# Kernel tuning notes

Measured on AMD Instinct MI355X. Metric: run time of the kernel, lower is better.

Reference implementation:

```python
import jax, jax.numpy as jnp
import numpy as np

HPC = 42  # HPC_FEATURES_LEN

def setup_inputs() -> dict:
    key = jax.random.key(0)
    ks = jax.random.split(key, 8)
    B, N, C, P, S = 4, 16384, 103, 2048, 32
    xyz = jax.random.normal(ks[0], (B, N, 3), dtype=jnp.float32)
    features = jax.random.normal(ks[1], (B, C, N), dtype=jnp.float32)
    new_xyz = jax.random.normal(ks[2], (B, P, 3), dtype=jnp.float32)
    idx = jax.random.randint(ks[3], (B, P, S), 0, N, dtype=jnp.int32)
    # 1x1-conv weights (out_ch, in_ch); gate conv sees full 3+C=106 channels
    Wg = jax.random.normal(ks[4], (64, 106), dtype=jnp.float32) * 0.05
    bg = jnp.zeros((64,), dtype=jnp.float32)
    W1 = jax.random.normal(ks[5], (64, 64), dtype=jnp.float32) * 0.05
    b1 = jnp.zeros((64,), dtype=jnp.float32)
    W2 = jax.random.normal(ks[6], (128, 64), dtype=jnp.float32) * 0.05
    b2 = jnp.zeros((128,), dtype=jnp.float32)
    W3 = jax.random.normal(ks[7], (256, 128), dtype=jnp.float32) * 0.05
    b3 = jnp.zeros((256,), dtype=jnp.float32)
    return {"xyz": xyz, "features": features, "new_xyz": new_xyz, "idx": idx,
            "Wg": Wg, "bg": bg, "W1": W1, "b1": b1, "W2": W2, "b2": b2,
            "W3": W3, "b3": b3}

def reference(xyz, features, new_xyz, idx, Wg, bg, W1, b1, W2, b2, W3, b3):
    # --- grouping: gather neighbors, center xyz, concat features ---
    # grouped_xyz: (B, P, S, 3) -> (B, 3, P, S)
    grouped_xyz = jax.vmap(lambda x, i: x[i])(xyz, idx) - new_xyz[:, :, None, :]
    grouped_xyz = jnp.transpose(grouped_xyz, (0, 3, 1, 2))
    # grouped_feat: (B, C, P, S)
    grouped_feat = jax.vmap(lambda f, i: f[:, i])(features, idx)
    nf = jnp.concatenate([grouped_xyz, grouped_feat], axis=1)  # (B, 3+C, P, S)
    base = nf[:, :-HPC]                                        # (B, 3+C-42, P, S)
    # --- gating 1x1 conv on full channels, then elementwise gate ---
    w = jnp.einsum('bcps,oc->bops', nf, Wg) + bg[None, :, None, None]
    x = base * (1.0 + w)
    # --- 1x1-conv MLP stack with ReLU ---
    for W, b in ((W1, b1), (W2, b2), (W3, b3)):
        x = jax.nn.relu(jnp.einsum('bcps,oc->bops', x, W) + b[None, :, None, None])
    # --- max pool over nsample ---
    pooled = jnp.max(x, axis=-1)  # (B, 256, P)
    return new_xyz, pooled
```

## Files before the change

### kernel.cpp

```cpp
#include <hip/hip_runtime.h>
#include <stdint.h>


namespace {
constexpr int kB = 4, kN = 16384, kC = 103, kP = 2048, kS = 32;

using short8 = __attribute__((ext_vector_type(8))) short;
using short4 = __attribute__((ext_vector_type(4))) short;
using f32x4  = __attribute__((ext_vector_type(4))) float;

constexpr int WG_HI = 0,     WG_LO = 8192;
constexpr int W1_HI = 16384, W1_LO = 20480;
constexpr int W2_HI = 24576, W2_LO = 32768;
constexpr int W3_HI = 40960, W3_LO = 73728;
constexpr size_t FT_OFF    = 262144;
constexpr size_t FT_SHORTS = (size_t)kB * kN * 128;
constexpr size_t WS_NEED   = FT_OFF + 2 * FT_SHORTS * 2;

__device__ __forceinline__ unsigned short f2bf(float x) {
    unsigned u = __float_as_uint(x);
    u += 0x7fffu + ((u >> 16) & 1u);
    return (unsigned short)(u >> 16);
}
__device__ __forceinline__ float bf2f(unsigned short h) {
    return __uint_as_float((unsigned)h << 16);
}

__global__ void copy_newxyz(const float* __restrict__ src, float* __restrict__ dst, int n) {
    int i = blockIdx.x * blockDim.x + threadIdx.x;
    if (i < n) dst[i] = src[i];
}

__global__ void prep_weights(const float* __restrict__ Wg, const float* __restrict__ W1,
                             const float* __restrict__ W2, const float* __restrict__ W3,
                             short* __restrict__ ws) {
    int i = blockIdx.x * blockDim.x + threadIdx.x;
    if (i >= 53248) return;
    float w; int hi, lo, j;
    if (i < 8192)       { j = i;         int o = j >> 7, c = j & 127; w = (c < 106) ? Wg[o * 106 + c] : 0.f; hi = WG_HI; lo = WG_LO; }
    else if (i < 12288) { j = i - 8192;  int o = j >> 6, c = j & 63;  w = W1[o * 64 + c];  hi = W1_HI; lo = W1_LO; }
    else if (i < 20480) { j = i - 12288; int o = j >> 6, c = j & 63;  w = W2[o * 64 + c];  hi = W2_HI; lo = W2_LO; }
    else                { j = i - 20480; int o = j >> 7, c = j & 127; w = W3[o * 128 + c]; hi = W3_HI; lo = W3_LO; }
    unsigned short h = f2bf(w);
    ws[hi + j] = (short)h;
    ws[lo + j] = (short)f2bf(w - bf2f(h));
}

__global__ __launch_bounds__(512) void prep_feat(const float* __restrict__ f,
                                                 short* __restrict__ ftH, short* __restrict__ ftL) {
    __shared__ float tile[kC][65];
    const int bb = blockIdx.x >> 8;
    const int n0 = (blockIdx.x & 255) * 64;
    const int tid = threadIdx.x;
    for (int c = tid >> 6; c < kC; c += 8)
        tile[c][tid & 63] = f[((size_t)bb * kC + c) * kN + n0 + (tid & 63)];
    __syncthreads();
    const int np = tid >> 3, gc = tid & 7;
    short* rH = ftH + ((size_t)bb * kN + n0 + np) * 128;
    short* rL = ftL + ((size_t)bb * kN + n0 + np) * 128;
    #pragma unroll
    for (int kk = 0; kk < 2; ++kk) {
        const int chunk = gc + 8 * kk;
        union { uint4 u; short s[8]; } H, L;
        #pragma unroll
        for (int e = 0; e < 8; ++e) {
            const int col = chunk * 8 + e;
            float v = (col >= 3 && col < 106) ? tile[col - 3][np] : 0.f;
            unsigned short hh = f2bf(v);
            H.s[e] = (short)hh;
            L.s[e] = (short)f2bf(v - bf2f(hh));
        }
        *(uint4*)(rH + chunk * 8) = H.u;
        *(uint4*)(rL + chunk * 8) = L.u;
    }
}

template<int NOT, int NPT, int KT, int LDC>
__device__ __forceinline__ void gemm_stage(
    const short* __restrict__ xh, const short* __restrict__ xl,
    const short* __restrict__ wh, const short* __restrict__ wl,
    const float* __restrict__ bias,
    int ot0, int pt0t, int lane, f32x4 (&acc)[NOT][NPT])
{
    const int q = lane >> 4, n16 = lane & 15;
    #pragma unroll
    for (int i = 0; i < NOT; ++i) {
        const f32x4 binit = *(const f32x4*)(bias + (ot0 + i) * 16 + 4 * q);
        #pragma unroll
        for (int j = 0; j < NPT; ++j) acc[i][j] = binit;
    }
    #pragma unroll
    for (int kt = 0; kt < KT; ++kt) {
        const int k0 = kt * 32 + q * 8;
        short8 bh[NPT], bl[NPT];
        #pragma unroll
        for (int j = 0; j < NPT; ++j) {
            const int p = (pt0t + j) * 16 + n16;
            const int e = p * LDC + (k0 ^ ((p & 7) << 3));
            bh[j] = *(const short8*)(xh + e);
            bl[j] = *(const short8*)(xl + e);
        }
        #pragma unroll
        for (int i = 0; i < NOT; ++i) {
            const size_t we = (size_t)((ot0 + i) * 16 + n16) * (KT * 32) + k0;
            const short8 ah = *(const short8*)(wh + we);
            const short8 al = *(const short8*)(wl + we);
            #pragma unroll
            for (int j = 0; j < NPT; ++j) {
                acc[i][j] = __builtin_amdgcn_mfma_f32_16x16x32_bf16(ah, bh[j], acc[i][j], 0, 0, 0);
                acc[i][j] = __builtin_amdgcn_mfma_f32_16x16x32_bf16(ah, bl[j], acc[i][j], 0, 0, 0);
                acc[i][j] = __builtin_amdgcn_mfma_f32_16x16x32_bf16(al, bh[j], acc[i][j], 0, 0, 0);
            }
        }
    }
}

template<int NOT, int NPT, bool GATE, int LDCO>
__device__ __forceinline__ void store_act(
    f32x4 (&acc)[NOT][NPT], short* __restrict__ oh, short* __restrict__ ol,
    const short* __restrict__ nfh, const short* __restrict__ nfl,
    int ot0, int pt0t, int lane)
{
    const int q = lane >> 4, n16 = lane & 15;
    #pragma unroll
    for (int i = 0; i < NOT; ++i) {
        const int ob = (ot0 + i) * 16 + 4 * q;
        #pragma unroll
        for (int j = 0; j < NPT; ++j) {
            const int p = (pt0t + j) * 16 + n16;
            const int cs = ob ^ ((p & 7) << 3);
            float v[4];
            #pragma unroll
            for (int r = 0; r < 4; ++r) v[r] = acc[i][j][r];
            if (GATE) {
                const short4 h4 = *(const short4*)(nfh + p * 128 + cs);
                const short4 l4 = *(const short4*)(nfl + p * 128 + cs);
                #pragma unroll
                for (int r = 0; r < 4; ++r) {
                    const float base = bf2f((unsigned short)h4[r]) + bf2f((unsigned short)l4[r]);
                    v[r] = fmaf(base, v[r], base);
                }
            } else {
                #pragma unroll
                for (int r = 0; r < 4; ++r) v[r] = fmaxf(v[r], 0.f);
            }
            short4 h4o, l4o;
            #pragma unroll
            for (int r = 0; r < 4; ++r) {
                const unsigned short h = f2bf(v[r]);
                h4o[r] = (short)h;
                l4o[r] = (short)f2bf(v[r] - bf2f(h));
            }
            *(short4*)(oh + p * LDCO + cs) = h4o;
            *(short4*)(ol + p * LDCO + cs) = l4o;
        }
    }
}

template<bool DENSE>
__global__ __launch_bounds__(512, 4) void pointnet_sa(
    const float* __restrict__ xyz, const float* __restrict__ features,
    const float* __restrict__ new_xyz, const int* __restrict__ idx,
    const short* __restrict__ ws, const short* __restrict__ ftH, const short* __restrict__ ftL,
    const float* __restrict__ bg, const float* __restrict__ b1,
    const float* __restrict__ b2, const float* __restrict__ b3,
    float* __restrict__ out_pooled)
{
    __shared__ short smem[32768];
    short* NFh = smem;          short* NFl = smem + 8192;
    short* X0h = smem + 16384;  short* X0l = smem + 20480;
    short* X1h = smem + 24576;  short* X1l = smem + 28672;
    short* X2h = NFh;           short* X2l = NFl;

    const int tid = threadIdx.x, lane = tid & 63, wave = tid >> 6;
    const int q = lane >> 4, n16 = lane & 15;
    const int pt0 = blockIdx.x * 64;
    const int b = pt0 >> 16;

    if (DENSE) {
        const int gp = tid >> 3, gc = tid & 7;
        const int pt = pt0 + gp;
        const int n = idx[pt];
        const short* rH = ftH + ((size_t)b * kN + n) * 128;
        const short* rL = ftL + ((size_t)b * kN + n) * 128;
        uint4 hc0 = *(const uint4*)(rH + gc * 8);
        uint4 hc1 = *(const uint4*)(rH + gc * 8 + 64);
        uint4 lc0 = *(const uint4*)(rL + gc * 8);
        uint4 lc1 = *(const uint4*)(rL + gc * 8 + 64);
        if (gc == 0) {
            const float* xp = xyz + ((size_t)b * kN + n) * 3;
            const int pp = (pt >> 5) & (kP - 1);
            const float* np = new_xyz + ((size_t)b * kP + pp) * 3;
            union { uint4 u; short s[8]; } H, L;
            H.u = hc0; L.u = lc0;
            #pragma unroll
            for (int c = 0; c < 3; ++c) {
                const float v = xp[c] - np[c];
                const unsigned short hh = f2bf(v);
                H.s[c] = (short)hh;
                L.s[c] = (short)f2bf(v - bf2f(hh));
            }
            hc0 = H.u; lc0 = L.u;
        }
        const int sw = (gc ^ (gp & 7)) * 8;
        *(uint4*)(NFh + gp * 128 + sw)      = hc0;
        *(uint4*)(NFh + gp * 128 + sw + 64) = hc1;
        *(uint4*)(NFl + gp * 128 + sw)      = lc0;
        *(uint4*)(NFl + gp * 128 + sw + 64) = lc1;
    } else {
        const int p = tid & 63;
        const int cg = tid >> 6;
        const int pt = pt0 + p;
        const int n = idx[pt];
        const int pp = (pt >> 5) & (kP - 1);
        const float* fb = features + (size_t)b * kC * kN + n;
        const float* xp = xyz + ((size_t)b * kN + n) * 3;
        const float* np = new_xyz + ((size_t)b * kP + pp) * 3;
        for (int c = cg; c < 128; c += 8) {
            float v;
            if (c < 3)        v = xp[c] - np[c];
            else if (c < 106) v = fb[(size_t)(c - 3) * kN];
            else              v = 0.f;
            const unsigned short h = f2bf(v);
            const int cs = c ^ ((p & 7) << 3);
            NFh[p * 128 + cs] = (short)h;
            NFl[p * 128 + cs] = (short)f2bf(v - bf2f(h));
        }
    }
    __syncthreads();

    {
        f32x4 acc[1][2];
        gemm_stage<1, 2, 4, 128>(NFh, NFl, ws + WG_HI, ws + WG_LO, bg,
                                 wave & 3, 2 * (wave >> 2), lane, acc);
        store_act<1, 2, true, 64>(acc, X0h, X0l, NFh, NFl, wave & 3, 2 * (wave >> 2), lane);
    }
    __syncthreads();

    {
        f32x4 acc[1][2];
        gemm_stage<1, 2, 2, 64>(X0h, X0l, ws + W1_HI, ws + W1_LO, b1,
                                wave & 3, 2 * (wave >> 2), lane, acc);
        store_act<1, 2, false, 64>(acc, X1h, X1l, nullptr, nullptr, wave & 3, 2 * (wave >> 2), lane);
    }
    __syncthreads();

    {
        f32x4 acc[2][2];
        gemm_stage<2, 2, 2, 64>(X1h, X1l, ws + W2_HI, ws + W2_LO, b2,
                                2 * (wave & 3), 2 * (wave >> 2), lane, acc);
        store_act<2, 2, false, 128>(acc, X2h, X2l, nullptr, nullptr, 2 * (wave & 3), 2 * (wave >> 2), lane);
    }
    __syncthreads();

    {
        f32x4 acc[2][4];
        gemm_stage<2, 4, 4, 128>(X2h, X2l, ws + W3_HI, ws + W3_LO, b3,
                                 2 * wave, 0, lane, acc);
        #pragma unroll
        for (int i = 0; i < 2; ++i) {
            #pragma unroll
            for (int sg = 0; sg < 2; ++sg) {
                #pragma unroll
                for (int r = 0; r < 4; ++r) {
                    float a = fmaxf(acc[i][2 * sg][r], acc[i][2 * sg + 1][r]);
                    a = fmaxf(a, __shfl_xor(a, 1, 16));
                    a = fmaxf(a, __shfl_xor(a, 2, 16));
                    a = fmaxf(a, __shfl_xor(a, 4, 16));
                    a = fmaxf(a, __shfl_xor(a, 8, 16));
                    a = fmaxf(a, 0.f);
                    if (n16 == 0) {
                        const int o = (2 * wave + i) * 16 + 4 * q + r;
                        const int g = (pt0 >> 5) + sg;
                        out_pooled[((size_t)(g >> 11) * 256 + o) * kP + (g & (kP - 1))] = a;
                    }
                }
            }
        }
    }
}
}

extern "C" void kernel_launch(void* const* d_in, const int* in_sizes, int n_in,
                              void* d_out, int out_size, void* d_ws, size_t ws_size,
                              hipStream_t stream) {
    const float* xyz      = (const float*)d_in[0];
    const float* features = (const float*)d_in[1];
    const float* new_xyz  = (const float*)d_in[2];
    const int*   idx      = (const int*)d_in[3];
    const float* Wg = (const float*)d_in[4];
    const float* bg = (const float*)d_in[5];
    const float* W1 = (const float*)d_in[6];
    const float* b1 = (const float*)d_in[7];
    const float* W2 = (const float*)d_in[8];
    const float* b2 = (const float*)d_in[9];
    const float* W3 = (const float*)d_in[10];
    const float* b3 = (const float*)d_in[11];
    float* out = (float*)d_out;
    short* ws  = (short*)d_ws;
    short* ftH = (short*)((char*)d_ws + FT_OFF);
    short* ftL = ftH + FT_SHORTS;

    const int nxyz = kB * kP * 3;
    copy_newxyz<<<(nxyz + 255) / 256, 256, 0, stream>>>(new_xyz, out, nxyz);
    prep_weights<<<(53248 + 255) / 256, 256, 0, stream>>>(Wg, W1, W2, W3, ws);

    float* pooled = out + nxyz;
    if (ws_size >= WS_NEED) {
        prep_feat<<<kB * (kN / 64), 512, 0, stream>>>(features, ftH, ftL);
        pointnet_sa<true><<<(kB * kP * kS) / 64, 512, 0, stream>>>(
            xyz, features, new_xyz, idx, ws, ftH, ftL, bg, b1, b2, b3, pooled);
    } else {
        pointnet_sa<false><<<(kB * kP * kS) / 64, 512, 0, stream>>>(
            xyz, features, new_xyz, idx, ws, nullptr, nullptr, bg, b1, b2, b3, pooled);
    }
}
```

Before: 185.9 us.

## Pipeline neighbor gathers via direct-to-LDS loads across multiple tiles per block

```diff
diff --git a/kernel.cpp b/kernel.cpp
--- a/kernel.cpp
+++ b/kernel.cpp
@@ -2,8 +2,12 @@
 #include <stdint.h>
 
 
+#define AS1 __attribute__((address_space(1)))
+#define AS3 __attribute__((address_space(3)))
+
 namespace {
 constexpr int kB = 4, kN = 16384, kC = 103, kP = 2048, kS = 32;
+constexpr int TPB = 4;
 
 using short8 = __attribute__((ext_vector_type(8))) short;
 using short4 = __attribute__((ext_vector_type(4))) short;
@@ -24,6 +28,14 @@
 }
 __device__ __forceinline__ float bf2f(unsigned short h) {
     return __uint_as_float((unsigned)h << 16);
+}
+
+__device__ __forceinline__ void glds16(const short* g, short* l) {
+    __builtin_amdgcn_global_load_lds((const AS1 unsigned int*)g, (AS3 unsigned int*)l, 16, 0, 0);
+}
+__device__ __forceinline__ void wg_barrier() {
+    asm volatile("s_waitcnt lgkmcnt(0)" ::: "memory");
+    __builtin_amdgcn_s_barrier();
 }
 
 __global__ void copy_newxyz(const float* __restrict__ src, float* __restrict__ dst, int n) {
@@ -111,6 +123,36 @@
                 acc[i][j] = __builtin_amdgcn_mfma_f32_16x16x32_bf16(ah, bl[j], acc[i][j], 0, 0, 0);
                 acc[i][j] = __builtin_amdgcn_mfma_f32_16x16x32_bf16(al, bh[j], acc[i][j], 0, 0, 0);
             }
+        }
+    }
+}
+
+template<int NPT, int KT, int LDC>
+__device__ __forceinline__ void gemm_pre(
+    const short* __restrict__ xh, const short* __restrict__ xl,
+    const short8* ah, const short8* al, const float* __restrict__ bias,
+    int ot0, int pt0t, int lane, f32x4 (&acc)[1][NPT])
+{
+    const int q = lane >> 4, n16 = lane & 15;
+    const f32x4 binit = *(const f32x4*)(bias + ot0 * 16 + 4 * q);
+    #pragma unroll
+    for (int j = 0; j < NPT; ++j) acc[0][j] = binit;
+    #pragma unroll
+    for (int kt = 0; kt < KT; ++kt) {
+        const int k0 = kt * 32 + q * 8;
+        short8 bh[NPT], bl[NPT];
+        #pragma unroll
+        for (int j = 0; j < NPT; ++j) {
+            const int p = (pt0t + j) * 16 + n16;
+            const int e = p * LDC + (k0 ^ ((p & 7) << 3));
+            bh[j] = *(const short8*)(xh + e);
+            bl[j] = *(const short8*)(xl + e);
+        }
+        #pragma unroll
+        for (int j = 0; j < NPT; ++j) {
+            acc[0][j] = __builtin_amdgcn_mfma_f32_16x16x32_bf16(ah[kt], bh[j], acc[0][j], 0, 0, 0);
+            acc[0][j] = __builtin_amdgcn_mfma_f32_16x16x32_bf16(ah[kt], bl[j], acc[0][j], 0, 0, 0);
+            acc[0][j] = __builtin_amdgcn_mfma_f32_16x16x32_bf16(al[kt], bh[j], acc[0][j], 0, 0, 0);
         }
     }
 }
@@ -157,16 +199,180 @@
     }
 }
 
-template<bool DENSE>
-__global__ __launch_bounds__(512, 4) void pointnet_sa(
-    const float* __restrict__ xyz, const float* __restrict__ features,
-    const float* __restrict__ new_xyz, const int* __restrict__ idx,
+__global__ __launch_bounds__(512, 4) void pointnet_sa_pipe(
+    const float* __restrict__ xyz, const float* __restrict__ new_xyz,
+    const int* __restrict__ idx,
     const short* __restrict__ ws, const short* __restrict__ ftH, const short* __restrict__ ftL,
     const float* __restrict__ bg, const float* __restrict__ b1,
     const float* __restrict__ b2, const float* __restrict__ b3,
     float* __restrict__ out_pooled)
 {
-    __shared__ short smem[32768];
+    __shared__ alignas(16) short smem[32768];
+    __shared__ alignas(16) float biasL[512];
+    short* NFh = smem;          short* NFl = smem + 8192;
+    short* X0h = smem + 16384;  short* X0l = smem + 20480;
+    short* X1h = smem + 24576;  short* X1l = smem + 28672;
+    short* X2h = smem + 16384;  short* X2l = smem + 24576;
+
+    const int tid = threadIdx.x, lane = tid & 63, wave = tid >> 6;
+    const int q = lane >> 4, n16 = lane & 15;
+    const int base = blockIdx.x * (64 * TPB);
+    const int b = base >> 16;
+    const size_t fb = (size_t)b * kN * 128;
+
+    biasL[tid] = (tid < 64) ? bg[tid] : (tid < 128) ? b1[tid - 64]
+               : (tid < 256) ? b2[tid - 128] : b3[tid - 256];
+
+    short8 w1h2[2], w1l2[2];
+    {
+        const int row = (wave & 3) * 16 + n16;
+        #pragma unroll
+        for (int kt = 0; kt < 2; ++kt) {
+            w1h2[kt] = *(const short8*)(ws + W1_HI + row * 64 + kt * 32 + q * 8);
+            w1l2[kt] = *(const short8*)(ws + W1_LO + row * 64 + kt * 32 + q * 8);
+        }
+    }
+
+    {
+        const int r0 = wave * 8 + (lane >> 4);
+        const int n0 = idx[base + r0];
+        const int n1 = idx[base + r0 + 4];
+        const int c0 = ((lane & 15) ^ (lane >> 4)) * 8;
+        const int c1 = ((lane & 15) ^ (4 + (lane >> 4))) * 8;
+        const int l0 = __builtin_amdgcn_readfirstlane(wave * 1024);
+        glds16(ftH + fb + (size_t)n0 * 128 + c0, smem + l0);
+        glds16(ftH + fb + (size_t)n1 * 128 + c1, smem + l0 + 512);
+        glds16(ftL + fb + (size_t)n0 * 128 + c0, smem + 8192 + l0);
+        glds16(ftL + fb + (size_t)n1 * 128 + c1, smem + 8192 + l0 + 512);
+    }
+    float xr0 = 0, xr1 = 0, xr2 = 0, nx0 = 0, nx1 = 0, nx2 = 0;
+    if ((lane & 7) == 0) {
+        const int p = wave * 8 + (lane >> 3);
+        const int n = idx[base + p];
+        const float* xp = xyz + ((size_t)b * kN + n) * 3;
+        const int pp = ((base + p) >> 5) & (kP - 1);
+        const float* np = new_xyz + ((size_t)b * kP + pp) * 3;
+        xr0 = xp[0]; xr1 = xp[1]; xr2 = xp[2];
+        nx0 = np[0]; nx1 = np[1]; nx2 = np[2];
+    }
+    __syncthreads();
+    if ((lane & 7) == 0) {
+        const int p = wave * 8 + (lane >> 3);
+        const int o = p * 128 + (p & 7) * 8;
+        float xd[3] = { xr0 - nx0, xr1 - nx1, xr2 - nx2 };
+        #pragma unroll
+        for (int c = 0; c < 3; ++c) {
+            const unsigned short h = f2bf(xd[c]);
+            NFh[o + c] = (short)h;
+            NFl[o + c] = (short)f2bf(xd[c] - bf2f(h));
+        }
+    }
+    wg_barrier();
+
+    for (int t = 0; t < TPB; ++t) {
+        const int tb = base + t * 64;
+        int ni0 = 0, ni1 = 0, nxy = 0;
+        if (t + 1 < TPB) {
+            const int r0 = wave * 8 + (lane >> 4);
+            ni0 = idx[tb + 64 + r0];
+            ni1 = idx[tb + 64 + r0 + 4];
+            if ((lane & 7) == 0) nxy = idx[tb + 64 + wave * 8 + (lane >> 3)];
+        }
+
+        {
+            f32x4 a0[1][2];
+            gemm_stage<1, 2, 4, 128>(NFh, NFl, ws + WG_HI, ws + WG_LO, biasL,
+                                     wave & 3, 2 * (wave >> 2), lane, a0);
+            store_act<1, 2, true, 64>(a0, X0h, X0l, NFh, NFl, wave & 3, 2 * (wave >> 2), lane);
+        }
+        wg_barrier();
+
+        if (t + 1 < TPB) {
+            const int c0 = ((lane & 15) ^ (lane >> 4)) * 8;
+            const int c1 = ((lane & 15) ^ (4 + (lane >> 4))) * 8;
+            const int l0 = __builtin_amdgcn_readfirstlane(wave * 1024);
+            glds16(ftH + fb + (size_t)ni0 * 128 + c0, smem + l0);
+            glds16(ftH + fb + (size_t)ni1 * 128 + c1, smem + l0 + 512);
+            glds16(ftL + fb + (size_t)ni0 * 128 + c0, smem + 8192 + l0);
+            glds16(ftL + fb + (size_t)ni1 * 128 + c1, smem + 8192 + l0 + 512);
+            if ((lane & 7) == 0) {
+                const int p = wave * 8 + (lane >> 3);
+                const float* xp = xyz + ((size_t)b * kN + nxy) * 3;
+                const int pp = ((tb + 64 + p) >> 5) & (kP - 1);
+                const float* np = new_xyz + ((size_t)b * kP + pp) * 3;
+                xr0 = xp[0]; xr1 = xp[1]; xr2 = xp[2];
+                nx0 = np[0]; nx1 = np[1]; nx2 = np[2];
+            }
+        }
+
+        {
+            f32x4 a1[1][2];
+            gemm_pre<2, 2, 64>(X0h, X0l, w1h2, w1l2, biasL + 64,
+                               wave & 3, 2 * (wave >> 2), lane, a1);
+            store_act<1, 2, false, 64>(a1, X1h, X1l, nullptr, nullptr,
+                                       wave & 3, 2 * (wave >> 2), lane);
+        }
+        wg_barrier();
+
+        f32x4 a2[2][2];
+        gemm_stage<2, 2, 2, 64>(X1h, X1l, ws + W2_HI, ws + W2_LO, biasL + 128,
+                                2 * (wave & 3), 2 * (wave >> 2), lane, a2);
+        wg_barrier();
+        store_act<2, 2, false, 128>(a2, X2h, X2l, nullptr, nullptr,
+                                    2 * (wave & 3), 2 * (wave >> 2), lane);
+        wg_barrier();
+
+        {
+            f32x4 a3[2][4];
+            gemm_stage<2, 4, 4, 128>(X2h, X2l, ws + W3_HI, ws + W3_LO, biasL + 256,
+                                     2 * wave, 0, lane, a3);
+            #pragma unroll
+            for (int i = 0; i < 2; ++i)
+                #pragma unroll
+                for (int sg = 0; sg < 2; ++sg)
+                    #pragma unroll
+                    for (int r = 0; r < 4; ++r) {
+                        float a = fmaxf(a3[i][2 * sg][r], a3[i][2 * sg + 1][r]);
+                        a = fmaxf(a, __shfl_xor(a, 1, 16));
+                        a = fmaxf(a, __shfl_xor(a, 2, 16));
+                        a = fmaxf(a, __shfl_xor(a, 4, 16));
+                        a = fmaxf(a, __shfl_xor(a, 8, 16));
+                        a = fmaxf(a, 0.f);
+                        if (n16 == 0) {
+                            const int o = (2 * wave + i) * 16 + 4 * q + r;
+                            const int g = (tb >> 5) + sg;
+                            out_pooled[((size_t)(g >> 11) * 256 + o) * kP + (g & (kP - 1))] = a;
+                        }
+                    }
+        }
+
+        if (t + 1 < TPB) {
+            asm volatile("s_waitcnt vmcnt(0)" ::: "memory");
+            if ((lane & 7) == 0) {
+                const int p = wave * 8 + (lane >> 3);
+                const int o = p * 128 + (p & 7) * 8;
+                float xd[3] = { xr0 - nx0, xr1 - nx1, xr2 - nx2 };
+                #pragma unroll
+                for (int c = 0; c < 3; ++c) {
+                    const unsigned short h = f2bf(xd[c]);
+                    NFh[o + c] = (short)h;
+                    NFl[o + c] = (short)f2bf(xd[c] - bf2f(h));
+                }
+            }
+            wg_barrier();
+        }
+    }
+}
+
+__global__ __launch_bounds__(512, 4) void pointnet_sa_scalar(
+    const float* __restrict__ xyz, const float* __restrict__ features,
+    const float* __restrict__ new_xyz, const int* __restrict__ idx,
+    const short* __restrict__ ws,
+    const float* __restrict__ bg, const float* __restrict__ b1,
+    const float* __restrict__ b2, const float* __restrict__ b3,
+    float* __restrict__ out_pooled)
+{
+    __shared__ alignas(16) short smem[32768];
     short* NFh = smem;          short* NFl = smem + 8192;
     short* X0h = smem + 16384;  short* X0l = smem + 20480;
     short* X1h = smem + 24576;  short* X1l = smem + 28672;
@@ -177,49 +383,19 @@
     const int pt0 = blockIdx.x * 64;
     const int b = pt0 >> 16;
 
-    if (DENSE) {
-        const int gp = tid >> 3, gc = tid & 7;
-        const int pt = pt0 + gp;
-        const int n = idx[pt];
-        const short* rH = ftH + ((size_t)b * kN + n) * 128;
-        const short* rL = ftL + ((size_t)b * kN + n) * 128;
-        uint4 hc0 = *(const uint4*)(rH + gc * 8);
-        uint4 hc1 = *(const uint4*)(rH + gc * 8 + 64);
-        uint4 lc0 = *(const uint4*)(rL + gc * 8);
-        uint4 lc1 = *(const uint4*)(rL + gc * 8 + 64);
-        if (gc == 0) {
-            const float* xp = xyz + ((size_t)b * kN + n) * 3;
-            const int pp = (pt >> 5) & (kP - 1);
-            const float* np = new_xyz + ((size_t)b * kP + pp) * 3;
-            union { uint4 u; short s[8]; } H, L;
-            H.u = hc0; L.u = lc0;
-            #pragma unroll
-            for (int c = 0; c < 3; ++c) {
-                const float v = xp[c] - np[c];
-                const unsigned short hh = f2bf(v);
-                H.s[c] = (short)hh;
-                L.s[c] = (short)f2bf(v - bf2f(hh));
-            }
-            hc0 = H.u; lc0 = L.u;
-        }
-        const int sw = (gc ^ (gp & 7)) * 8;
-        *(uint4*)(NFh + gp * 128 + sw)      = hc0;
-        *(uint4*)(NFh + gp * 128 + sw + 64) = hc1;
-        *(uint4*)(NFl + gp * 128 + sw)      = lc0;
-        *(uint4*)(NFl + gp * 128 + sw + 64) = lc1;
-    } else {
+    {
         const int p = tid & 63;
         const int cg = tid >> 6;
         const int pt = pt0 + p;
         const int n = idx[pt];
         const int pp = (pt >> 5) & (kP - 1);
-        const float* fb = features + (size_t)b * kC * kN + n;
+        const float* fbp = features + (size_t)b * kC * kN + n;
         const float* xp = xyz + ((size_t)b * kN + n) * 3;
         const float* np = new_xyz + ((size_t)b * kP + pp) * 3;
         for (int c = cg; c < 128; c += 8) {
             float v;
             if (c < 3)        v = xp[c] - np[c];
-            else if (c < 106) v = fb[(size_t)(c - 3) * kN];
+            else if (c < 106) v = fbp[(size_t)(c - 3) * kN];
             else              v = 0.f;
             const unsigned short h = f2bf(v);
             const int cs = c ^ ((p & 7) << 3);
@@ -228,7 +404,6 @@
         }
     }
     __syncthreads();
-
     {
         f32x4 acc[1][2];
         gemm_stage<1, 2, 4, 128>(NFh, NFl, ws + WG_HI, ws + WG_LO, bg,
@@ -236,7 +411,6 @@
         store_act<1, 2, true, 64>(acc, X0h, X0l, NFh, NFl, wave & 3, 2 * (wave >> 2), lane);
     }
     __syncthreads();
-
     {
         f32x4 acc[1][2];
         gemm_stage<1, 2, 2, 64>(X0h, X0l, ws + W1_HI, ws + W1_LO, b1,
@@ -244,7 +418,6 @@
         store_act<1, 2, false, 64>(acc, X1h, X1l, nullptr, nullptr, wave & 3, 2 * (wave >> 2), lane);
     }
     __syncthreads();
-
     {
         f32x4 acc[2][2];
         gemm_stage<2, 2, 2, 64>(X1h, X1l, ws + W2_HI, ws + W2_LO, b2,
@@ -252,15 +425,14 @@
         store_act<2, 2, false, 128>(acc, X2h, X2l, nullptr, nullptr, 2 * (wave & 3), 2 * (wave >> 2), lane);
     }
     __syncthreads();
-
     {
         f32x4 acc[2][4];
         gemm_stage<2, 4, 4, 128>(X2h, X2l, ws + W3_HI, ws + W3_LO, b3,
                                  2 * wave, 0, lane, acc);
         #pragma unroll
-        for (int i = 0; i < 2; ++i) {
+        for (int i = 0; i < 2; ++i)
             #pragma unroll
-            for (int sg = 0; sg < 2; ++sg) {
+            for (int sg = 0; sg < 2; ++sg)
                 #pragma unroll
                 for (int r = 0; r < 4; ++r) {
                     float a = fmaxf(acc[i][2 * sg][r], acc[i][2 * sg + 1][r]);
@@ -275,8 +447,6 @@
                         out_pooled[((size_t)(g >> 11) * 256 + o) * kP + (g & (kP - 1))] = a;
                     }
                 }
-            }
-        }
     }
 }
 }
@@ -308,10 +478,10 @@
     float* pooled = out + nxyz;
     if (ws_size >= WS_NEED) {
         prep_feat<<<kB * (kN / 64), 512, 0, stream>>>(features, ftH, ftL);
-        pointnet_sa<true><<<(kB * kP * kS) / 64, 512, 0, stream>>>(
-            xyz, features, new_xyz, idx, ws, ftH, ftL, bg, b1, b2, b3, pooled);
+        pointnet_sa_pipe<<<(kB * kP * kS) / 64 / TPB, 512, 0, stream>>>(
+            xyz, new_xyz, idx, ws, ftH, ftL, bg, b1, b2, b3, pooled);
     } else {
-        pointnet_sa<false><<<(kB * kP * kS) / 64, 512, 0, stream>>>(
-            xyz, features, new_xyz, idx, ws, nullptr, nullptr, bg, b1, b2, b3, pooled);
-    }
-}
+        pointnet_sa_scalar<<<(kB * kP * kS) / 64, 512, 0, stream>>>(
+            xyz, features, new_xyz, idx, ws, bg, b1, b2, b3, pooled);
+    }
+}
```

New measurement: 280.6 us. +50.9%, slower.

## Shrink shared-memory footprint by aliasing activation buffers to fit more blocks

Applied to the files above, without the earlier changes.

```diff
diff --git a/kernel.cpp b/kernel.cpp
--- a/kernel.cpp
+++ b/kernel.cpp
@@ -75,19 +75,21 @@
     }
 }
 
-template<int NOT, int NPT, int KT, int LDC>
-__device__ __forceinline__ void gemm_stage(
+template<int NOT, int NPT, int KT, int LDC, int LDW, bool INIT>
+__device__ __forceinline__ void gemm_core(
     const short* __restrict__ xh, const short* __restrict__ xl,
     const short* __restrict__ wh, const short* __restrict__ wl,
-    const float* __restrict__ bias,
+    const float* __restrict__ bias, int kwoff,
     int ot0, int pt0t, int lane, f32x4 (&acc)[NOT][NPT])
 {
     const int q = lane >> 4, n16 = lane & 15;
-    #pragma unroll
-    for (int i = 0; i < NOT; ++i) {
-        const f32x4 binit = *(const f32x4*)(bias + (ot0 + i) * 16 + 4 * q);
-        #pragma unroll
-        for (int j = 0; j < NPT; ++j) acc[i][j] = binit;
+    if constexpr (INIT) {
+        #pragma unroll
+        for (int i = 0; i < NOT; ++i) {
+            const f32x4 binit = *(const f32x4*)(bias + (ot0 + i) * 16 + 4 * q);
+            #pragma unroll
+            for (int j = 0; j < NPT; ++j) acc[i][j] = binit;
+        }
     }
     #pragma unroll
     for (int kt = 0; kt < KT; ++kt) {
@@ -102,7 +104,7 @@
         }
         #pragma unroll
         for (int i = 0; i < NOT; ++i) {
-            const size_t we = (size_t)((ot0 + i) * 16 + n16) * (KT * 32) + k0;
+            const size_t we = (size_t)((ot0 + i) * 16 + n16) * LDW + kwoff + k0;
             const short8 ah = *(const short8*)(wh + we);
             const short8 al = *(const short8*)(wl + we);
             #pragma unroll
@@ -158,7 +160,7 @@
 }
 
 template<bool DENSE>
-__global__ __launch_bounds__(512, 4) void pointnet_sa(
+__global__ __launch_bounds__(512, 3) void pointnet_sa(
     const float* __restrict__ xyz, const float* __restrict__ features,
     const float* __restrict__ new_xyz, const int* __restrict__ idx,
     const short* __restrict__ ws, const short* __restrict__ ftH, const short* __restrict__ ftL,
@@ -166,11 +168,11 @@
     const float* __restrict__ b2, const float* __restrict__ b3,
     float* __restrict__ out_pooled)
 {
-    __shared__ short smem[32768];
-    short* NFh = smem;          short* NFl = smem + 8192;
-    short* X0h = smem + 16384;  short* X0l = smem + 20480;
-    short* X1h = smem + 24576;  short* X1l = smem + 28672;
-    short* X2h = NFh;           short* X2l = NFl;
+    __shared__ alignas(16) short smem[24576];
+    short* NFh = smem;
+    short* NFl = smem + 8192;
+    short* X0h = smem + 16384;
+    short* X0l = smem + 20480;
 
     const int tid = threadIdx.x, lane = tid & 63, wave = tid >> 6;
     const int q = lane >> 4, n16 = lane & 15;
@@ -213,13 +215,13 @@
         const int pt = pt0 + p;
         const int n = idx[pt];
         const int pp = (pt >> 5) & (kP - 1);
-        const float* fb = features + (size_t)b * kC * kN + n;
+        const float* fbp = features + (size_t)b * kC * kN + n;
         const float* xp = xyz + ((size_t)b * kN + n) * 3;
         const float* np = new_xyz + ((size_t)b * kP + pp) * 3;
         for (int c = cg; c < 128; c += 8) {
             float v;
             if (c < 3)        v = xp[c] - np[c];
-            else if (c < 106) v = fb[(size_t)(c - 3) * kN];
+            else if (c < 106) v = fbp[(size_t)(c - 3) * kN];
             else              v = 0.f;
             const unsigned short h = f2bf(v);
             const int cs = c ^ ((p & 7) << 3);
@@ -230,49 +232,57 @@
     __syncthreads();
 
     {
-        f32x4 acc[1][2];
-        gemm_stage<1, 2, 4, 128>(NFh, NFl, ws + WG_HI, ws + WG_LO, bg,
-                                 wave & 3, 2 * (wave >> 2), lane, acc);
-        store_act<1, 2, true, 64>(acc, X0h, X0l, NFh, NFl, wave & 3, 2 * (wave >> 2), lane);
+        f32x4 a[1][2];
+        gemm_core<1, 2, 4, 128, 128, true>(NFh, NFl, ws + WG_HI, ws + WG_LO, bg, 0,
+                                           wave & 3, 2 * (wave >> 2), lane, a);
+        store_act<1, 2, true, 64>(a, X0h, X0l, NFh, NFl, wave & 3, 2 * (wave >> 2), lane);
     }
     __syncthreads();
 
     {
-        f32x4 acc[1][2];
-        gemm_stage<1, 2, 2, 64>(X0h, X0l, ws + W1_HI, ws + W1_LO, b1,
-                                wave & 3, 2 * (wave >> 2), lane, acc);
-        store_act<1, 2, false, 64>(acc, X1h, X1l, nullptr, nullptr, wave & 3, 2 * (wave >> 2), lane);
+        f32x4 a[1][2];
+        gemm_core<1, 2, 2, 64, 64, true>(X0h, X0l, ws + W1_HI, ws + W1_LO, b1, 0,
+                                         wave & 3, 2 * (wave >> 2), lane, a);
+        store_act<1, 2, false, 128>(a, NFh, NFl, nullptr, nullptr,
+                                    wave & 3, 2 * (wave >> 2), lane);
     }
     __syncthreads();
 
     {
-        f32x4 acc[2][2];
-        gemm_stage<2, 2, 2, 64>(X1h, X1l, ws + W2_HI, ws + W2_LO, b2,
-                                2 * (wave & 3), 2 * (wave >> 2), lane, acc);
-        store_act<2, 2, false, 128>(acc, X2h, X2l, nullptr, nullptr, 2 * (wave & 3), 2 * (wave >> 2), lane);
+        f32x4 a[2][2];
+        gemm_core<2, 2, 2, 128, 64, true>(NFh, NFl, ws + W2_HI, ws + W2_LO, b2, 0,
+                                          2 * (wave & 3), 2 * (wave >> 2), lane, a);
+        if ((wave & 3) < 2)
+            store_act<2, 2, false, 64>(a, X0h, X0l, nullptr, nullptr,
+                                       2 * (wave & 3), 2 * (wave >> 2), lane);
+        else
+            store_act<2, 2, false, 128>(a, NFh + 64, NFl + 64, nullptr, nullptr,
+                                        (2 * (wave & 3)) & 3, 2 * (wave >> 2), lane);
     }
     __syncthreads();
 
     {
-        f32x4 acc[2][4];
-        gemm_stage<2, 4, 4, 128>(X2h, X2l, ws + W3_HI, ws + W3_LO, b3,
-                                 2 * wave, 0, lane, acc);
+        f32x4 a[2][4];
+        gemm_core<2, 4, 2, 64, 128, true >(X0h, X0l, ws + W3_HI, ws + W3_LO, b3, 0,
+                                           2 * wave, 0, lane, a);
+        gemm_core<2, 4, 2, 128, 128, false>(NFh + 64, NFl + 64, ws + W3_HI, ws + W3_LO,
+                                            nullptr, 64, 2 * wave, 0, lane, a);
         #pragma unroll
         for (int i = 0; i < 2; ++i) {
             #pragma unroll
             for (int sg = 0; sg < 2; ++sg) {
                 #pragma unroll
                 for (int r = 0; r < 4; ++r) {
-                    float a = fmaxf(acc[i][2 * sg][r], acc[i][2 * sg + 1][r]);
-                    a = fmaxf(a, __shfl_xor(a, 1, 16));
-                    a = fmaxf(a, __shfl_xor(a, 2, 16));
-                    a = fmaxf(a, __shfl_xor(a, 4, 16));
-                    a = fmaxf(a, __shfl_xor(a, 8, 16));
-                    a = fmaxf(a, 0.f);
+                    float v = fmaxf(a[i][2 * sg][r], a[i][2 * sg + 1][r]);
+                    v = fmaxf(v, __shfl_xor(v, 1, 16));
+                    v = fmaxf(v, __shfl_xor(v, 2, 16));
+                    v = fmaxf(v, __shfl_xor(v, 4, 16));
+                    v = fmaxf(v, __shfl_xor(v, 8, 16));
+                    v = fmaxf(v, 0.f);
                     if (n16 == 0) {
                         const int o = (2 * wave + i) * 16 + 4 * q + r;
                         const int g = (pt0 >> 5) + sg;
-                        out_pooled[((size_t)(g >> 11) * 256 + o) * kP + (g & (kP - 1))] = a;
+                        out_pooled[((size_t)(g >> 11) * 256 + o) * kP + (g & (kP - 1))] = v;
                     }
                 }
             }
```

After: 184.8 us. No clear change (-0.6%).
